# Optimization experiments

Measured on AMD Instinct MI355X. Metric: run time of the kernel, lower is better.

The kernel has to match this reference:

```python
import jax, jax.numpy as jnp
import numpy as np

D, H, F, L = 3, 3, 2048, 12  # d_model, nhead, dim_feedforward (torch default), num_layers
EPS = 1e-5


def _ln(x, w, b):
    m = x.mean(-1, keepdims=True)
    v = ((x - m) ** 2).mean(-1, keepdims=True)
    return (x - m) / jnp.sqrt(v + EPS) * w + b


def _mha(q_in, k_in, v_in, w, b, ow, ob):
    # w: [3D, D] packed qkv in_proj (torch layout), x: [T, B, D] seq-first
    qw, kw, vw = w[:D], w[D:2 * D], w[2 * D:]
    qb, kb, vb = b[:D], b[D:2 * D], b[2 * D:]
    q = q_in @ qw.T + qb
    k = k_in @ kw.T + kb
    v = v_in @ vw.T + vb
    hd = D // H  # head_dim = 1
    qh = q.reshape(q.shape[0], q.shape[1], H, hd)
    kh = k.reshape(k.shape[0], k.shape[1], H, hd)
    vh = v.reshape(v.shape[0], v.shape[1], H, hd)
    scores = jnp.einsum('qbhd,kbhd->bhqk', qh, kh) / np.sqrt(hd)
    attn = jax.nn.softmax(scores, axis=-1)
    o = jnp.einsum('bhqk,kbhd->qbhd', attn, vh).reshape(q_in.shape)
    return o @ ow.T + ob


def _encode(x, p):
    # post-norm TransformerEncoderLayer x12, then final encoder LayerNorm
    for i in range(L):
        x = _ln(x + _mha(x, x, x, p['sa_w'][i], p['sa_b'][i], p['sa_ow'][i], p['sa_ob'][i]),
                p['n1_w'][i], p['n1_b'][i])
        h = jax.nn.relu(x @ p['l1_w'][i].T + p['l1_b'][i]) @ p['l2_w'][i].T + p['l2_b'][i]
        x = _ln(x + h, p['n2_w'][i], p['n2_b'][i])
    return _ln(x, p['nf_w'], p['nf_b'])


def _decode(x, mem, p):
    # post-norm TransformerDecoderLayer x12 (no masks, matching the source), final LayerNorm
    for i in range(L):
        x = _ln(x + _mha(x, x, x, p['sa_w'][i], p['sa_b'][i], p['sa_ow'][i], p['sa_ob'][i]),
                p['n1_w'][i], p['n1_b'][i])
        x = _ln(x + _mha(x, mem, mem, p['ca_w'][i], p['ca_b'][i], p['ca_ow'][i], p['ca_ob'][i]),
                p['n2_w'][i], p['n2_b'][i])
        h = jax.nn.relu(x @ p['l1_w'][i].T + p['l1_b'][i]) @ p['l2_w'][i].T + p['l2_b'][i]
        x = _ln(x + h, p['n3_w'][i], p['n3_b'][i])
    return _ln(x, p['nf_w'], p['nf_b'])


def setup_inputs() -> dict:
    key = jax.random.key(0)
    ks = iter(jax.random.split(key, 64))

    def rn(shape, scale=0.1):
        return jax.random.normal(next(ks), shape, jnp.float32) * scale

    B, C, T = 16, 2, 32
    inp = {'src': rn((B, C, T), 1.0), 'angle': rn((B,), 1.0)}
    inp.update(dict(
        enc_sa_w=rn((L, 3 * D, D)), enc_sa_b=rn((L, 3 * D)), enc_sa_ow=rn((L, D, D)), enc_sa_ob=rn((L, D)),
        enc_l1_w=rn((L, F, D)), enc_l1_b=rn((L, F)), enc_l2_w=rn((L, D, F)), enc_l2_b=rn((L, D)),
        enc_n1_w=jnp.ones((L, D)), enc_n1_b=jnp.zeros((L, D)),
        enc_n2_w=jnp.ones((L, D)), enc_n2_b=jnp.zeros((L, D)),
        enc_nf_w=jnp.ones((D,)), enc_nf_b=jnp.zeros((D,)),
        dec_sa_w=rn((L, 3 * D, D)), dec_sa_b=rn((L, 3 * D)), dec_sa_ow=rn((L, D, D)), dec_sa_ob=rn((L, D)),
        dec_ca_w=rn((L, 3 * D, D)), dec_ca_b=rn((L, 3 * D)), dec_ca_ow=rn((L, D, D)), dec_ca_ob=rn((L, D)),
        dec_l1_w=rn((L, F, D)), dec_l1_b=rn((L, F)), dec_l2_w=rn((L, D, F)), dec_l2_b=rn((L, D)),
        dec_n1_w=jnp.ones((L, D)), dec_n1_b=jnp.zeros((L, D)),
        dec_n2_w=jnp.ones((L, D)), dec_n2_b=jnp.zeros((L, D)),
        dec_n3_w=jnp.ones((L, D)), dec_n3_b=jnp.zeros((L, D)),
        dec_nf_w=jnp.ones((D,)), dec_nf_b=jnp.zeros((D,)),
    ))
    return inp


def reference(src, angle,
              enc_sa_w, enc_sa_b, enc_sa_ow, enc_sa_ob, enc_l1_w, enc_l1_b, enc_l2_w, enc_l2_b,
              enc_n1_w, enc_n1_b, enc_n2_w, enc_n2_b, enc_nf_w, enc_nf_b,
              dec_sa_w, dec_sa_b, dec_sa_ow, dec_sa_ob, dec_ca_w, dec_ca_b, dec_ca_ow, dec_ca_ob,
              dec_l1_w, dec_l1_b, dec_l2_w, dec_l2_b,
              dec_n1_w, dec_n1_b, dec_n2_w, dec_n2_b, dec_n3_w, dec_n3_b, dec_nf_w, dec_nf_b):
    enc = dict(sa_w=enc_sa_w, sa_b=enc_sa_b, sa_ow=enc_sa_ow, sa_ob=enc_sa_ob,
               l1_w=enc_l1_w, l1_b=enc_l1_b, l2_w=enc_l2_w, l2_b=enc_l2_b,
               n1_w=enc_n1_w, n1_b=enc_n1_b, n2_w=enc_n2_w, n2_b=enc_n2_b,
               nf_w=enc_nf_w, nf_b=enc_nf_b)
    dec = dict(sa_w=dec_sa_w, sa_b=dec_sa_b, sa_ow=dec_sa_ow, sa_ob=dec_sa_ob,
               ca_w=dec_ca_w, ca_b=dec_ca_b, ca_ow=dec_ca_ow, ca_ob=dec_ca_ob,
               l1_w=dec_l1_w, l1_b=dec_l1_b, l2_w=dec_l2_w, l2_b=dec_l2_b,
               n1_w=dec_n1_w, n1_b=dec_n1_b, n2_w=dec_n2_w, n2_b=dec_n2_b,
               n3_w=dec_n3_w, n3_b=dec_n3_b, nf_w=dec_nf_w, nf_b=dec_nf_b)
    B, _, T = src.shape
    ang = jnp.broadcast_to(angle.reshape(B, 1, 1), (B, 1, T))
    s = jnp.concatenate([src, ang], axis=1)       # [B, 3, T]
    s = jnp.transpose(s, (2, 0, 1))                # [T, B, 3] seq-first
    mem = _encode(s, enc)                          # encoder depends only on src: compute once
    out0 = jnp.zeros_like(s).at[0].set(s[0])

    def step(out, t):
        pred = _decode(out, mem, dec)              # full no-mask decoder, as in the torch loop
        return out.at[t].set(pred[t]), None

    out, _ = jax.lax.scan(step, out0, jnp.arange(1, T))
    return jnp.transpose(out, (1, 2, 0))           # [B, 3, T]
```

## Files before the change

### kernel.cpp

```cpp
#include <hip/hip_runtime.h>
#include <math.h>

#define FF 2048
#define NL 12
#define NB 16
#define TT 32
#define EPS 1e-5f
#define LOG2E 1.44269504088896f

typedef float v2f __attribute__((ext_vector_type(2)));
__device__ __forceinline__ v2f mk2(float x){ v2f r; r.x = x; r.y = x; return r; }

__global__ __launch_bounds__(256) void prepack_kernel(
    const float* __restrict__ enc_l1_w, const float* __restrict__ enc_l1_b,
    const float* __restrict__ enc_l2_w,
    const float* __restrict__ dec_l1_w, const float* __restrict__ dec_l1_b,
    const float* __restrict__ dec_l2_w,
    float4* __restrict__ w_all)
{
    int idx = blockIdx.x * blockDim.x + threadIdx.x;
    if (idx >= 24 * 1024) return;
    int lay = idx >> 10;
    int fp  = idx & 1023;
    int f0  = 2*fp, f1 = 2*fp + 1;
    const float *w1, *b1, *w2;
    if (lay < NL) {
        w1 = enc_l1_w + (size_t)lay * FF * 3;
        b1 = enc_l1_b + (size_t)lay * FF;
        w2 = enc_l2_w + (size_t)lay * 3 * FF;
    } else {
        int l = lay - NL;
        w1 = dec_l1_w + (size_t)l * FF * 3;
        b1 = dec_l1_b + (size_t)l * FF;
        w2 = dec_l2_w + (size_t)l * 3 * FF;
    }
    float4* base = w_all + (size_t)lay * 4096;
    base[fp]        = make_float4(w1[f0*3+0], w1[f1*3+0], w1[f0*3+1], w1[f1*3+1]);
    base[1024 + fp] = make_float4(w1[f0*3+2], w1[f1*3+2], b1[f0],     b1[f1]);
    base[2048 + fp] = make_float4(w2[f0],     w2[f1],     w2[FF+f0],  w2[FF+f1]);
    base[3072 + fp] = make_float4(w2[2*FF+f0], w2[2*FF+f1], 0.f, 0.f);
}

struct __align__(16) SharedMem {
    float4 wbuf[2][4096];
    float4 x4[TT];
    float4 fred[TT][3];
    float4 outst[TT];
    float4 mem4[TT];
    float  kk[3][TT];
    float  vv[3][TT];
    float  oo[TT][3];
    float  ck[NL][3][TT];
    float  cv[NL][3][TT];
};

__device__ __forceinline__ void ln3s(float y0, float y1, float y2,
    const float* __restrict__ w, const float* __restrict__ b,
    float& o0, float& o1, float& o2)
{
    float m  = (y0 + y1 + y2) * (1.0f / 3.0f);
    float d0 = y0 - m, d1 = y1 - m, d2 = y2 - m;
    float v  = (d0*d0 + d1*d1 + d2*d2) * (1.0f / 3.0f);
    float r  = __builtin_amdgcn_rsqf(v + EPS);
    o0 = d0 * r * w[0] + b[0];
    o1 = d1 * r * w[1] + b[1];
    o2 = d2 * r * w[2] + b[2];
}

template<int CTRL>
__device__ __forceinline__ float dpp_add(float v)
{
    int sh = __builtin_amdgcn_update_dpp(0, __float_as_int(v), CTRL, 0xF, 0xF, true);
    return v + __int_as_float(sh);
}

__device__ __forceinline__ float wave_sum64(float v)
{
    v = dpp_add<0x111>(v);
    v = dpp_add<0x112>(v);
    v = dpp_add<0x114>(v);
    v = dpp_add<0x118>(v);
    v = dpp_add<0x142>(v);
    v = dpp_add<0x143>(v);
    return v;
}

__device__ __forceinline__ float sum4(float4 r)
{
    return (r.x + r.y) + (r.z + r.w);
}

template<bool MASK>
__device__ __forceinline__ float attn_half(float qs,
    const float* __restrict__ k, const float* __restrict__ v,
    int half, int ntok, int rep, float repw)
{
    const float4* k4 = (const float4*)k;
    const float4* v4 = (const float4*)v;
    float den = 0.f, nv = 0.f;
    #pragma unroll
    for (int jb = 0; jb < 4; ++jb) {
        float4 kq = k4[half*4 + jb];
        float4 vq = v4[half*4 + jb];
        const float kj[4] = {kq.x, kq.y, kq.z, kq.w};
        const float vj[4] = {vq.x, vq.y, vq.z, vq.w};
        #pragma unroll
        for (int u = 0; u < 4; ++u) {
            float w = exp2f(qs * kj[u]);
            if (MASK) {
                const int j = half*16 + jb*4 + u;
                w = (j < ntok) ? w : 0.f;
                w = (j == rep) ? w * repw : w;
            }
            den += w;
            nv = fmaf(w, vj[u], nv);
        }
    }
    den += __shfl_xor(den, 32, 64);
    nv  += __shfl_xor(nv , 32, 64);
    return nv * __builtin_amdgcn_rcpf(den);
}

template<int NII>
__device__ __forceinline__ void ffn_body(SharedMem& s, int tid,
    const float4* __restrict__ wb)
{
    const int flane = tid & 255;
    const int g     = tid >> 8;
    const int w4    = (tid >> 6) & 3;
    const int lane  = tid & 63;
    const v2f z2 = {0.f, 0.f};
    float X0[NII], X1[NII], X2[NII];
    v2f ac0[NII], ac1[NII], ac2[NII];
    #pragma unroll
    for (int ii = 0; ii < NII; ++ii) {
        float4 xt = s.x4[g + 4*ii];
        X0[ii] = xt.x; X1[ii] = xt.y; X2[ii] = xt.z;
        ac0[ii] = z2; ac1[ii] = z2; ac2[ii] = z2;
    }
    #pragma unroll
    for (int jp = 0; jp < 4; ++jp) {
        const int fp = flane + 256*jp;
        float4 A0 = wb[fp], A1 = wb[1024+fp];
        float4 C0 = wb[2048+fp], C1 = wb[3072+fp];
        v2f ax = {A0.x, A0.y}, ay = {A0.z, A0.w};
        v2f az = {A1.x, A1.y}, ab = {A1.z, A1.w};
        v2f cx = {C0.x, C0.y}, cy = {C0.z, C0.w};
        v2f cz = {C1.x, C1.y};
        #pragma unroll
        for (int ii = 0; ii < NII; ++ii) {
            v2f h2 = __builtin_elementwise_fma(ax, mk2(X0[ii]),
                     __builtin_elementwise_fma(ay, mk2(X1[ii]),
                     __builtin_elementwise_fma(az, mk2(X2[ii]), ab)));
            h2 = __builtin_elementwise_max(h2, z2);
            ac0[ii] = __builtin_elementwise_fma(cx, h2, ac0[ii]);
            ac1[ii] = __builtin_elementwise_fma(cy, h2, ac1[ii]);
            ac2[ii] = __builtin_elementwise_fma(cz, h2, ac2[ii]);
        }
    }
    #pragma unroll
    for (int ii = 0; ii < NII; ++ii) {
        const int t = g + 4*ii;
        float r0 = wave_sum64(ac0[ii].x + ac0[ii].y);
        float r1 = wave_sum64(ac1[ii].x + ac1[ii].y);
        float r2 = wave_sum64(ac2[ii].x + ac2[ii].y);
        if (lane == 63) {
            ((float*)&s.fred[t][0])[w4] = r0;
            ((float*)&s.fred[t][1])[w4] = r1;
            ((float*)&s.fred[t][2])[w4] = r2;
        }
    }
}

template<bool HAS_CA, bool MASK_SA>
__device__ __forceinline__ void run_layer(SharedMem& s, int tid,
    int ntok, int rep, float repw, int do_combine, int p,
    const float4* __restrict__ nw,
    const float* __restrict__ saw, const float* __restrict__ sab,
    const float* __restrict__ saow, const float* __restrict__ saob,
    const float* __restrict__ n1w, const float* __restrict__ n1b,
    const float* __restrict__ caw, const float* __restrict__ cab,
    const float* __restrict__ caow, const float* __restrict__ caob,
    const float* __restrict__ n2w, const float* __restrict__ n2b,
    const float* __restrict__ ckh, const float* __restrict__ cvh,
    const float* __restrict__ pl2b, const float* __restrict__ pnw,
    const float* __restrict__ pnb)
{
    const int wv   = tid >> 6;
    const int lane = tid & 63;
    const int q    = lane & 31;
    const int half = lane >> 5;
    float X0 = 0.f, X1 = 0.f, X2 = 0.f;

    if (wv >= 3) {
        for (int k = tid - 192; k < 4096; k += 832)
            s.wbuf[p ^ 1][k] = nw[k];
    } else {
        const int h = wv;
        float4 xa = s.x4[q];
        if (do_combine) {
            float f0 = sum4(s.fred[q][0]);
            float f1 = sum4(s.fred[q][1]);
            float f2 = sum4(s.fred[q][2]);
            ln3s(xa.x + f0 + pl2b[0], xa.y + f1 + pl2b[1],
                 xa.z + f2 + pl2b[2], pnw, pnb, X0, X1, X2);
        } else { X0 = xa.x; X1 = xa.y; X2 = xa.z; }
        if (lane < 32 && q < ntok) {
            s.kk[h][q] = sab[3+h] + saw[9+3*h]*X0  + saw[10+3*h]*X1 + saw[11+3*h]*X2;
            s.vv[h][q] = sab[6+h] + saw[18+3*h]*X0 + saw[19+3*h]*X1 + saw[20+3*h]*X2;
        }
        float qv = (sab[h] + saw[3*h]*X0 + saw[3*h+1]*X1 + saw[3*h+2]*X2) * LOG2E;
        float o = attn_half<MASK_SA>(qv, s.kk[h], s.vv[h], half, ntok, rep, repw);
        if (lane < 32 && q < ntok) s.oo[q][h] = o;
    }
    __syncthreads();
    if (wv == 0 && lane < 32 && q < ntok) {
        float o0 = s.oo[q][0], o1 = s.oo[q][1], o2 = s.oo[q][2];
        float y0 = X0 + saob[0] + saow[0]*o0 + saow[1]*o1 + saow[2]*o2;
        float y1 = X1 + saob[1] + saow[3]*o0 + saow[4]*o1 + saow[5]*o2;
        float y2 = X2 + saob[2] + saow[6]*o0 + saow[7]*o1 + saow[8]*o2;
        float a0, a1, a2;
        ln3s(y0, y1, y2, n1w, n1b, a0, a1, a2);
        s.x4[q] = make_float4(a0, a1, a2, 0.f);
    }
    __syncthreads();
    if (HAS_CA) {
        float xb0 = 0.f, xb1 = 0.f, xb2 = 0.f;
        if (wv < 3) {
            const int h = wv;
            float4 xb = s.x4[q];
            xb0 = xb.x; xb1 = xb.y; xb2 = xb.z;
            float cqv = (cab[h] + caw[3*h]*xb0 + caw[3*h+1]*xb1 + caw[3*h+2]*xb2) * LOG2E;
            float o = attn_half<false>(cqv, ckh + h*TT, cvh + h*TT, half, TT, -1, 1.f);
            if (lane < 32 && q < ntok) s.oo[q][h] = o;
        }
        __syncthreads();
        if (wv == 0 && lane < 32 && q < ntok) {
            float o0 = s.oo[q][0], o1 = s.oo[q][1], o2 = s.oo[q][2];
            float y0 = xb0 + caob[0] + caow[0]*o0 + caow[1]*o1 + caow[2]*o2;
            float y1 = xb1 + caob[1] + caow[3]*o0 + caow[4]*o1 + caow[5]*o2;
            float y2 = xb2 + caob[2] + caow[6]*o0 + caow[7]*o1 + caow[8]*o2;
            float a0, a1, a2;
            ln3s(y0, y1, y2, n2w, n2b, a0, a1, a2);
            s.x4[q] = make_float4(a0, a1, a2, 0.f);
        }
        __syncthreads();
    }
    const float4* wb = s.wbuf[p];
    if (ntok <= 8)       ffn_body<2>(s, tid, wb);
    else if (ntok <= 16) ffn_body<4>(s, tid, wb);
    else                 ffn_body<8>(s, tid, wb);
    __syncthreads();
}

__global__ __launch_bounds__(1024, 4) void seq_kernel(
    const float* __restrict__ src, const float* __restrict__ angle,
    const float* __restrict__ enc_sa_w, const float* __restrict__ enc_sa_b,
    const float* __restrict__ enc_sa_ow, const float* __restrict__ enc_sa_ob,
    const float* __restrict__ enc_l2_b,
    const float* __restrict__ enc_n1_w, const float* __restrict__ enc_n1_b,
    const float* __restrict__ enc_n2_w, const float* __restrict__ enc_n2_b,
    const float* __restrict__ enc_nf_w, const float* __restrict__ enc_nf_b,
    const float* __restrict__ dec_sa_w, const float* __restrict__ dec_sa_b,
    const float* __restrict__ dec_sa_ow, const float* __restrict__ dec_sa_ob,
    const float* __restrict__ dec_ca_w, const float* __restrict__ dec_ca_b,
    const float* __restrict__ dec_ca_ow, const float* __restrict__ dec_ca_ob,
    const float* __restrict__ dec_l2_b,
    const float* __restrict__ dec_n1_w, const float* __restrict__ dec_n1_b,
    const float* __restrict__ dec_n2_w, const float* __restrict__ dec_n2_b,
    const float* __restrict__ dec_n3_w, const float* __restrict__ dec_n3_b,
    const float* __restrict__ dec_nf_w, const float* __restrict__ dec_nf_b,
    const float4* __restrict__ w_all,
    float* __restrict__ out)
{
    __shared__ SharedMem s;
    const int tid = threadIdx.x;
    const int b   = blockIdx.x;

    for (int k = tid; k < 4096; k += 1024)
        s.wbuf[0][k] = w_all[k];
    if (tid < TT) {
        float x0 = src[b*64 + tid];
        float x1 = src[b*64 + 32 + tid];
        float x2 = angle[b];
        s.x4[tid] = make_float4(x0, x1, x2, 0.f);
        if (tid == 0) s.outst[0] = make_float4(x0, x1, x2, 0.f);
    }
    __syncthreads();

    int lp = 0;
    for (int i = 0; i < NL; ++i) {
        const float4* nw = w_all + (size_t)((i < 11) ? (i + 1) : 12) * 4096;
        const int pi = (i > 0) ? (i - 1) : 0;
        run_layer<false, false>(s, tid, TT, -1, 1.f, i > 0, lp & 1, nw,
            enc_sa_w + i*27, enc_sa_b + i*9, enc_sa_ow + i*9, enc_sa_ob + i*3,
            enc_n1_w + i*3, enc_n1_b + i*3,
            nullptr, nullptr, nullptr, nullptr, nullptr, nullptr,
            nullptr, nullptr,
            enc_l2_b + pi*3, enc_n2_w + pi*3, enc_n2_b + pi*3);
        ++lp;
    }
    if (tid < 32) {
        float4 xa = s.x4[tid];
        float f0 = sum4(s.fred[tid][0]);
        float f1 = sum4(s.fred[tid][1]);
        float f2 = sum4(s.fred[tid][2]);
        float o0, o1, o2, m0, m1, m2;
        ln3s(xa.x + f0 + enc_l2_b[33], xa.y + f1 + enc_l2_b[34],
             xa.z + f2 + enc_l2_b[35], enc_n2_w + 33, enc_n2_b + 33, o0, o1, o2);
        ln3s(o0, o1, o2, enc_nf_w, enc_nf_b, m0, m1, m2);
        s.mem4[tid] = make_float4(m0, m1, m2, 0.f);
        s.x4[tid]   = (tid == 0) ? s.outst[0] : make_float4(0.f, 0.f, 0.f, 0.f);
    }
    __syncthreads();

    for (int idx = tid; idx < NL * 96; idx += 1024) {
        const int lyr = idx / 96;
        const int r   = idx - lyr * 96;
        const int hh  = r >> 5;
        const int t   = r & 31;
        const float* w  = dec_ca_w + lyr*27;
        const float* bb = dec_ca_b + lyr*9;
        float4 mr = s.mem4[t];
        s.ck[lyr][hh][t] = bb[3+hh] + w[(3+hh)*3]*mr.x + w[(3+hh)*3+1]*mr.y + w[(3+hh)*3+2]*mr.z;
        s.cv[lyr][hh][t] = bb[6+hh] + w[(6+hh)*3]*mr.x + w[(6+hh)*3+1]*mr.y + w[(6+hh)*3+2]*mr.z;
    }
    __syncthreads();

    for (int t = 1; t < TT; ++t) {
        const int ntok = t + 1;
        for (int i = 0; i < NL; ++i) {
            const float4* nw = w_all + (size_t)(12 + ((i < 11) ? (i + 1) : 0)) * 4096;
            const int pi = (i > 0) ? (i - 1) : 0;
            run_layer<true, true>(s, tid, ntok, t, (float)(TT - t), i > 0, lp & 1, nw,
                dec_sa_w + i*27, dec_sa_b + i*9, dec_sa_ow + i*9, dec_sa_ob + i*3,
                dec_n1_w + i*3, dec_n1_b + i*3,
                dec_ca_w + i*27, dec_ca_b + i*9, dec_ca_ow + i*9, dec_ca_ob + i*3,
                dec_n2_w + i*3, dec_n2_b + i*3,
                &s.ck[i][0][0], &s.cv[i][0][0],
                dec_l2_b + pi*3, dec_n3_w + pi*3, dec_n3_b + pi*3);
            ++lp;
        }
        if (tid < 32) {
            if (tid == 0) {
                float4 xa = s.x4[t];
                float f0 = sum4(s.fred[t][0]);
                float f1 = sum4(s.fred[t][1]);
                float f2 = sum4(s.fred[t][2]);
                float o0, o1, o2, p0, p1, p2;
                ln3s(xa.x + f0 + dec_l2_b[33], xa.y + f1 + dec_l2_b[34],
                     xa.z + f2 + dec_l2_b[35], dec_n3_w + 33, dec_n3_b + 33,
                     o0, o1, o2);
                ln3s(o0, o1, o2, dec_nf_w, dec_nf_b, p0, p1, p2);
                s.outst[t] = make_float4(p0, p1, p2, 0.f);
            }
            s.x4[tid] = (tid <= t) ? s.outst[tid] : make_float4(0.f, 0.f, 0.f, 0.f);
        }
        __syncthreads();
    }

    if (tid < TT) {
        float4 o = s.outst[tid];
        out[b*96 +  0 + tid] = o.x;
        out[b*96 + 32 + tid] = o.y;
        out[b*96 + 64 + tid] = o.z;
    }
}

extern "C" void kernel_launch(void* const* d_in, const int* in_sizes, int n_in,
                              void* d_out, int out_size, void* d_ws, size_t ws_size,
                              hipStream_t stream) {
    const float* src      = (const float*)d_in[0];
    const float* angle    = (const float*)d_in[1];
    const float* enc_sa_w = (const float*)d_in[2];
    const float* enc_sa_b = (const float*)d_in[3];
    const float* enc_sa_ow= (const float*)d_in[4];
    const float* enc_sa_ob= (const float*)d_in[5];
    const float* enc_l1_w = (const float*)d_in[6];
    const float* enc_l1_b = (const float*)d_in[7];
    const float* enc_l2_w = (const float*)d_in[8];
    const float* enc_l2_b = (const float*)d_in[9];
    const float* enc_n1_w = (const float*)d_in[10];
    const float* enc_n1_b = (const float*)d_in[11];
    const float* enc_n2_w = (const float*)d_in[12];
    const float* enc_n2_b = (const float*)d_in[13];
    const float* enc_nf_w = (const float*)d_in[14];
    const float* enc_nf_b = (const float*)d_in[15];
    const float* dec_sa_w = (const float*)d_in[16];
    const float* dec_sa_b = (const float*)d_in[17];
    const float* dec_sa_ow= (const float*)d_in[18];
    const float* dec_sa_ob= (const float*)d_in[19];
    const float* dec_ca_w = (const float*)d_in[20];
    const float* dec_ca_b = (const float*)d_in[21];
    const float* dec_ca_ow= (const float*)d_in[22];
    const float* dec_ca_ob= (const float*)d_in[23];
    const float* dec_l1_w = (const float*)d_in[24];
    const float* dec_l1_b = (const float*)d_in[25];
    const float* dec_l2_w = (const float*)d_in[26];
    const float* dec_l2_b = (const float*)d_in[27];
    const float* dec_n1_w = (const float*)d_in[28];
    const float* dec_n1_b = (const float*)d_in[29];
    const float* dec_n2_w = (const float*)d_in[30];
    const float* dec_n2_b = (const float*)d_in[31];
    const float* dec_n3_w = (const float*)d_in[32];
    const float* dec_n3_b = (const float*)d_in[33];
    const float* dec_nf_w = (const float*)d_in[34];
    const float* dec_nf_b = (const float*)d_in[35];

    float4* w_all = (float4*)d_ws;

    prepack_kernel<<<(24 * 1024 + 255) / 256, 256, 0, stream>>>(
        enc_l1_w, enc_l1_b, enc_l2_w,
        dec_l1_w, dec_l1_b, dec_l2_w,
        w_all);

    seq_kernel<<<NB, 1024, 0, stream>>>(
        src, angle,
        enc_sa_w, enc_sa_b, enc_sa_ow, enc_sa_ob, enc_l2_b,
        enc_n1_w, enc_n1_b, enc_n2_w, enc_n2_b, enc_nf_w, enc_nf_b,
        dec_sa_w, dec_sa_b, dec_sa_ow, dec_sa_ob,
        dec_ca_w, dec_ca_b, dec_ca_ow, dec_ca_ob, dec_l2_b,
        dec_n1_w, dec_n1_b, dec_n2_w, dec_n2_b, dec_n3_w, dec_n3_b,
        dec_nf_w, dec_nf_b,
        (const float4*)w_all,
        (float*)d_out);
}
```

Before: 2.066 ms.

## Fuse self-attn out-proj/LN into cross-attn phase and split weight prefetch

Each of the three head waves now redundantly computes the self-attention output projection and LayerNorm itself, then runs cross-attention directly. This removes one block-wide barrier and one shared-memory round trip per decoder layer. The next-layer weight prefetch by the spare waves is split across the two phases, and the softmax accumulation uses two independent partial sums to shorten dependency chains. The cost is duplicated per-wave arithmetic and an extra shared-memory buffer.

```diff
diff --git a/kernel.cpp b/kernel.cpp
--- a/kernel.cpp
+++ b/kernel.cpp
@@ -50,6 +50,7 @@
     float  kk[3][TT];
     float  vv[3][TT];
     float  oo[TT][3];
+    float  oo2[TT][3];
     float  ck[NL][3][TT];
     float  cv[NL][3][TT];
 };
@@ -97,7 +98,7 @@
 {
     const float4* k4 = (const float4*)k;
     const float4* v4 = (const float4*)v;
-    float den = 0.f, nv = 0.f;
+    float den0 = 0.f, den1 = 0.f, nv0 = 0.f, nv1 = 0.f;
     #pragma unroll
     for (int jb = 0; jb < 4; ++jb) {
         float4 kq = k4[half*4 + jb];
@@ -112,10 +113,12 @@
                 w = (j < ntok) ? w : 0.f;
                 w = (j == rep) ? w * repw : w;
             }
-            den += w;
-            nv = fmaf(w, vj[u], nv);
-        }
-    }
+            if (jb & 1) { den1 += w; nv1 = fmaf(w, vj[u], nv1); }
+            else        { den0 += w; nv0 = fmaf(w, vj[u], nv0); }
+        }
+    }
+    float den = den0 + den1;
+    float nv  = nv0 + nv1;
     den += __shfl_xor(den, 32, 64);
     nv  += __shfl_xor(nv , 32, 64);
     return nv * __builtin_amdgcn_rcpf(den);
@@ -191,9 +194,10 @@
     const int q    = lane & 31;
     const int half = lane >> 5;
     float X0 = 0.f, X1 = 0.f, X2 = 0.f;
+    float B0 = 0.f, B1 = 0.f, B2 = 0.f;
 
     if (wv >= 3) {
-        for (int k = tid - 192; k < 4096; k += 832)
+        for (int k = tid - 192; k < 2048; k += 832)
             s.wbuf[p ^ 1][k] = nw[k];
     } else {
         const int h = wv;
@@ -214,32 +218,32 @@
         if (lane < 32 && q < ntok) s.oo[q][h] = o;
     }
     __syncthreads();
-    if (wv == 0 && lane < 32 && q < ntok) {
+    if (wv >= 3) {
+        for (int k = 2048 + tid - 192; k < 4096; k += 832)
+            s.wbuf[p ^ 1][k] = nw[k];
+    } else {
+        const int h = wv;
         float o0 = s.oo[q][0], o1 = s.oo[q][1], o2 = s.oo[q][2];
         float y0 = X0 + saob[0] + saow[0]*o0 + saow[1]*o1 + saow[2]*o2;
         float y1 = X1 + saob[1] + saow[3]*o0 + saow[4]*o1 + saow[5]*o2;
         float y2 = X2 + saob[2] + saow[6]*o0 + saow[7]*o1 + saow[8]*o2;
-        float a0, a1, a2;
-        ln3s(y0, y1, y2, n1w, n1b, a0, a1, a2);
-        s.x4[q] = make_float4(a0, a1, a2, 0.f);
+        ln3s(y0, y1, y2, n1w, n1b, B0, B1, B2);
+        if (!HAS_CA) {
+            if (wv == 0 && lane < 32 && q < ntok)
+                s.x4[q] = make_float4(B0, B1, B2, 0.f);
+        } else {
+            float cqv = (cab[h] + caw[3*h]*B0 + caw[3*h+1]*B1 + caw[3*h+2]*B2) * LOG2E;
+            float oc = attn_half<false>(cqv, ckh + h*TT, cvh + h*TT, half, TT, -1, 1.f);
+            if (lane < 32 && q < ntok) s.oo2[q][h] = oc;
+        }
     }
     __syncthreads();
     if (HAS_CA) {
-        float xb0 = 0.f, xb1 = 0.f, xb2 = 0.f;
-        if (wv < 3) {
-            const int h = wv;
-            float4 xb = s.x4[q];
-            xb0 = xb.x; xb1 = xb.y; xb2 = xb.z;
-            float cqv = (cab[h] + caw[3*h]*xb0 + caw[3*h+1]*xb1 + caw[3*h+2]*xb2) * LOG2E;
-            float o = attn_half<false>(cqv, ckh + h*TT, cvh + h*TT, half, TT, -1, 1.f);
-            if (lane < 32 && q < ntok) s.oo[q][h] = o;
-        }
-        __syncthreads();
         if (wv == 0 && lane < 32 && q < ntok) {
-            float o0 = s.oo[q][0], o1 = s.oo[q][1], o2 = s.oo[q][2];
-            float y0 = xb0 + caob[0] + caow[0]*o0 + caow[1]*o1 + caow[2]*o2;
-            float y1 = xb1 + caob[1] + caow[3]*o0 + caow[4]*o1 + caow[5]*o2;
-            float y2 = xb2 + caob[2] + caow[6]*o0 + caow[7]*o1 + caow[8]*o2;
+            float c0 = s.oo2[q][0], c1 = s.oo2[q][1], c2 = s.oo2[q][2];
+            float y0 = B0 + caob[0] + caow[0]*c0 + caow[1]*c1 + caow[2]*c2;
+            float y1 = B1 + caob[1] + caow[3]*c0 + caow[4]*c1 + caow[5]*c2;
+            float y2 = B2 + caob[2] + caow[6]*c0 + caow[7]*c1 + caow[8]*c2;
             float a0, a1, a2;
             ln3s(y0, y1, y2, n2w, n2b, a0, a1, a2);
             s.x4[q] = make_float4(a0, a1, a2, 0.f);
```

New measurement: 2.043 ms. No clear change (-1.1%).
